# Kernel tuning notes

Measured on AMD Instinct MI355X. Metric: run time of the kernel, lower is better.

Reference implementation:

```python
import jax, jax.numpy as jnp
import numpy as np

GRID = 32            # grid_size -> num_locs = 1024
H, W = 8, 32         # ray panorama height/width
N_ANGLES = 360       # binned_rays: one bin per rounded degree


def _circ_conv(x, w, b, pad):
    # Conv2d with padding_mode='circular' (NCHW, OIHW)
    if pad > 0:
        x = jnp.pad(x, ((0, 0), (0, 0), (pad, pad), (pad, pad)), mode='wrap')
    y = jax.lax.conv_general_dilated(x, w, (1, 1), 'VALID',
                                     dimension_numbers=('NCHW', 'OIHW', 'NCHW'))
    return y + b[None, :, None, None]


def setup_inputs() -> dict:
    key = jax.random.key(0)
    ks = jax.random.split(key, 8)
    B, N, F, Co = 2, 20, 128, 64
    bbox = jax.random.uniform(ks[0], (B, 4), dtype=jnp.float32)
    near_locs = jax.random.uniform(ks[1], (B, N, 2), dtype=jnp.float32)
    near_feats = jax.random.normal(ks[2], (B, N, F, H, W), dtype=jnp.float32)
    overhead_feat = jax.random.normal(ks[3], (B, Co, GRID, GRID), dtype=jnp.float32)
    rays = jax.random.normal(ks[4], (N_ANGLES, 3, H, W), dtype=jnp.float32)
    cin = 8  # 1 dist + 3 orient + 2 pano stats + 2 overhead stats
    W1 = jax.random.normal(ks[5], (1, cin, 3, 3), dtype=jnp.float32) * 0.1
    b1 = jnp.zeros((1,), jnp.float32)
    W2 = jax.random.normal(ks[6], (1, cin, 5, 5), dtype=jnp.float32) * 0.1
    b2 = jnp.zeros((1,), jnp.float32)
    Wf = jax.random.normal(ks[7], (1, 2, 1, 1), dtype=jnp.float32) * 0.1
    bf = jnp.zeros((1,), jnp.float32)
    return dict(bbox=bbox, near_locs=near_locs, near_feats=near_feats,
                overhead_feat=overhead_feat, rays=rays,
                W1=W1, b1=b1, W2=W2, b2=b2, Wf=Wf, bf=bf)


def _grid_helper(bbox, near_locs):
    # grid-cell centers from bbox; D = euclidean dist, theta = bearing in [0, 2pi)
    ys = jnp.linspace(bbox[0], bbox[2], GRID)
    xs = jnp.linspace(bbox[1], bbox[3], GRID)
    gy, gx = jnp.meshgrid(ys, xs, indexing='ij')
    centers = jnp.stack([gy.ravel(), gx.ravel()], -1)              # [L,2]
    diff = near_locs[None, :, :] - centers[:, None, :]             # [L,N,2]
    D = jnp.sqrt(jnp.sum(diff * diff, -1))                         # [L,N]
    theta = jnp.mod(jnp.arctan2(diff[..., 1], diff[..., 0]), 2.0 * jnp.pi)
    return D, theta


def _one(bbox, near_locs, near_feats, overhead_feat, rays, W1, b1, W2, b2, Wf, bf):
    N, F = near_feats.shape[:2]
    L = GRID * GRID
    D, theta = _grid_helper(bbox, near_locs)
    theta_inds = jnp.mod(jnp.round(jnp.rad2deg(theta)).astype(jnp.int32), N_ANGLES)
    orientation = rays[theta_inds.reshape(-1)].reshape(L, N, 3, H, W)  # irregular gather
    distance = jnp.broadcast_to(D[:, :, None, None, None], (L, N, 1, H, W))
    # panorama stats: max/mean over channel dim of pano features
    pano_stats = jnp.stack([near_feats.max(1), near_feats.mean(1)], 1)  # [N,2,H,W]
    x_pano = jnp.broadcast_to(pano_stats[None], (L, N, 2, H, W))
    # overhead stats: flatten spatial -> (L, Co), max/mean over channels
    ov = overhead_feat.reshape(overhead_feat.shape[0], -1).T            # [L, Co]
    ov_stats = jnp.stack([ov.max(1), ov.mean(1)], 1)                    # [L,2]
    x_ov = jnp.broadcast_to(ov_stats[:, None, :, None, None], (L, N, 2, H, W))
    inp = jnp.concatenate([distance, orientation, x_pano, x_ov], 2)     # [L,N,8,H,W]
    x = inp.reshape(L * N, 8, H, W)
    c1 = _circ_conv(x, W1, b1, 1)
    c2 = _circ_conv(x, W2, b2, 2)
    fused = jnp.concatenate([c1, c2], 1)                                # [L*N,2,H,W]
    logits = _circ_conv(fused, Wf, bf, 0).reshape(L, N, H, W)
    weight = jax.nn.softmax(logits.reshape(L, -1), axis=1).reshape(L, N, H, W)
    tmp_feats = jnp.transpose(near_feats, (0, 2, 3, 1))                 # [N,H,W,F]
    grid_feats = jnp.einsum('pxyf,spxy->sf', tmp_feats, weight)         # [L,F]
    return (grid_feats.reshape(GRID, GRID, F),
            weight.reshape(GRID, GRID, N, H, W))


def reference(bbox, near_locs, near_feats, overhead_feat, rays, W1, b1, W2, b2, Wf, bf):
    fn = jax.vmap(_one, in_axes=(0, 0, 0, 0, None, None, None, None, None, None, None))
    return fn(bbox, near_locs, near_feats, overhead_feat, rays, W1, b1, W2, b2, Wf, bf)
```

## Files before the change

kernel.cpp:

```cpp
#include <hip/hip_runtime.h>
#include <hip/hip_fp16.h>
#include <math.h>

#define HH 8
#define WW 32
#define HW 256
#define NN 20
#define FF 128
#define LL 1024
#define AA 360
#define CO 64
#define KK 5120
#define KS 8
#define KC 640
#define BM 32
#define BK 64

#define OFF_LPANO      (AA*HW)
#define OFF_OV(B)      (OFF_LPANO + (B)*NN*HW)
#define OFF_SCAL(B)    (OFF_OV(B) + (B)*LL*2)
#define OFF_D(B)       (OFF_SCAL(B) + 8)
#define OFF_IDX(B)     (OFF_D(B) + (B)*LL*NN)
#define OFF_BASE2(B)   (OFF_IDX(B) + (B)*LL*NN)
#define OFF_MX(B)      (OFF_BASE2(B) + (B)*LL*NN)
#define OFF_INV(B)     (OFF_MX(B) + (B)*LL)
#define OFF_BT(B)      (((OFF_INV(B) + (B)*LL + 7)/8)*8)
#define OFF_CP(B)      (OFF_BT(B) + (B)*FF*KK/2)

typedef __attribute__((ext_vector_type(8))) _Float16 f16x8;
typedef __attribute__((ext_vector_type(4))) _Float16 f16x4;
typedef __attribute__((ext_vector_type(4))) float f32x4;

__global__ __launch_bounds__(256)
void kA_pre(const float* __restrict__ bbox, const float* __restrict__ locs,
            const float* __restrict__ rays, const float* __restrict__ feats,
            const float* __restrict__ overhead,
            const float* __restrict__ W1, const float* __restrict__ b1,
            const float* __restrict__ W2, const float* __restrict__ b2,
            const float* __restrict__ Wf, const float* __restrict__ bfp,
            float* __restrict__ ws, int B)
{
    const int bid = blockIdx.x, tid = threadIdx.x;
    const int g1 = AA + B*NN + B*4 + 1;
    const int gGeo = (B*LL*NN + 255)/256;

    if (bid < g1) {
        const float wf0 = Wf[0], wf1 = Wf[1];

        if (bid < AA) {
            __shared__ float s[3*HW];
            for (int c = 0; c < 3; ++c) s[c*HW + tid] = rays[(bid*3 + c)*HW + tid];
            __syncthreads();
            const int h = tid >> 5, w = tid & 31;
            float c1 = 0.f, c2 = 0.f;
            #pragma unroll
            for (int c = 0; c < 3; ++c) {
                #pragma unroll
                for (int ky = 0; ky < 3; ++ky)
                    #pragma unroll
                    for (int kx = 0; kx < 3; ++kx)
                        c1 += W1[(1+c)*9 + ky*3 + kx] *
                              s[c*HW + (((h+ky+7)&7)<<5) + ((w+kx+31)&31)];
                #pragma unroll
                for (int ky = 0; ky < 5; ++ky)
                    #pragma unroll
                    for (int kx = 0; kx < 5; ++kx)
                        c2 += W2[(1+c)*25 + ky*5 + kx] *
                              s[c*HW + (((h+ky+6)&7)<<5) + ((w+kx+30)&31)];
            }
            ws[bid*HW + tid] = wf0*c1 + wf1*c2;
            return;
        }

        const int pb = bid - AA;
        if (pb < B*NN) {
            __shared__ float p[2*HW];
            const float* fp = feats + (size_t)pb * FF * HW + tid;
            float mx = -INFINITY; double sm = 0.0;
            for (int f = 0; f < FF; ++f) {
                float v = fp[(size_t)f * HW];
                mx = fmaxf(mx, v); sm += (double)v;
            }
            p[tid]      = mx;
            p[HW + tid] = (float)(sm / 128.0);
            __syncthreads();
            const int h = tid >> 5, w = tid & 31;
            float c1 = 0.f, c2 = 0.f;
            #pragma unroll
            for (int c = 0; c < 2; ++c) {
                #pragma unroll
                for (int ky = 0; ky < 3; ++ky)
                    #pragma unroll
                    for (int kx = 0; kx < 3; ++kx)
                        c1 += W1[(4+c)*9 + ky*3 + kx] *
                              p[c*HW + (((h+ky+7)&7)<<5) + ((w+kx+31)&31)];
                #pragma unroll
                for (int ky = 0; ky < 5; ++ky)
                    #pragma unroll
                    for (int kx = 0; kx < 5; ++kx)
                        c2 += W2[(4+c)*25 + ky*5 + kx] *
                              p[c*HW + (((h+ky+6)&7)<<5) + ((w+kx+30)&31)];
            }
            ws[OFF_LPANO + pb*HW + tid] = wf0*c1 + wf1*c2;
            return;
        }

        const int ob = pb - B*NN;
        if (ob < B*4) {
            const int t = ob*256 + tid;
            const int b = t >> 10, l = t & 1023;
            const float* op = overhead + (size_t)b*CO*LL + l;
            float mx = -INFINITY; double sm = 0.0;
            for (int c = 0; c < CO; ++c) {
                float v = op[(size_t)c*LL];
                mx = fmaxf(mx, v); sm += (double)v;
            }
            ws[OFF_OV(B) + t*2]     = mx;
            ws[OFF_OV(B) + t*2 + 1] = (float)(sm / 64.0);
            return;
        }

        if (tid == 0) {
            double s10=0, s16=0, s17=0, s20=0, s26=0, s27=0;
            for (int i = 0; i < 9;  ++i) { s10 += W1[i]; s16 += W1[54+i];  s17 += W1[63+i]; }
            for (int i = 0; i < 25; ++i) { s20 += W2[i]; s26 += W2[150+i]; s27 += W2[175+i]; }
            ws[OFF_SCAL(B)+0] = (float)(wf0*s10 + wf1*s20);
            ws[OFF_SCAL(B)+1] = (float)(wf0*s16 + wf1*s26);
            ws[OFF_SCAL(B)+2] = (float)(wf0*s17 + wf1*s27);
            ws[OFF_SCAL(B)+3] = wf0*b1[0] + wf1*b2[0] + bfp[0];
        }
        return;
    }

    if (bid < g1 + gGeo) {
        const int t = (bid - g1)*256 + tid;
        if (t >= B*LL*NN) return;
        const int b = t / (LL*NN), r = t % (LL*NN), l = r / NN, n = r % NN;
        const int iy = l >> 5, ix = l & 31;
        const double y0 = (double)bbox[b*4+0], x0 = (double)bbox[b*4+1];
        const double y1 = (double)bbox[b*4+2], x1 = (double)bbox[b*4+3];
        const double cy = y0 + (double)iy * (y1 - y0) / 31.0;
        const double cx = x0 + (double)ix * (x1 - x0) / 31.0;
        const double d0 = (double)locs[(b*NN+n)*2+0] - cy;
        const double d1 = (double)locs[(b*NN+n)*2+1] - cx;
        const double D  = sqrt(d0*d0 + d1*d1);
        double th = atan2(d1, d0);
        const double TWO_PI = 6.283185307179586476925286766559;
        th -= TWO_PI * floor(th / TWO_PI);
        const double deg = th * 57.295779513082320876798154814105;
        int k = (int)llrint(deg);
        int idx = k % 360; if (idx < 0) idx += 360;
        ws[OFF_D(B) + t] = (float)D;
        ((int*)(ws + OFF_IDX(B)))[t] = idx;
        return;
    }

    {
        const int NG_PER_B = NN*FF*64;
        const int g = (bid - g1 - gGeo)*256 + tid;
        if (g >= B*NG_PER_B) return;
        const int b = g / NG_PER_B;
        const int r = g - b*NG_PER_B;
        const int n = r / (FF*64);
        const int r2 = r % (FF*64);
        const int f = r2 >> 6;
        const int hw0 = (r2 & 63) << 2;
        const float4 v = *(const float4*)(feats + ((size_t)((b*NN + n)*FF + f))*HW + hw0);
        f16x4 h;
        h[0] = (_Float16)v.x; h[1] = (_Float16)v.y;
        h[2] = (_Float16)v.z; h[3] = (_Float16)v.w;
        _Float16* bt = (_Float16*)(ws + OFF_BT(B));
        *(f16x4*)(bt + ((size_t)(b*FF + f))*KK + n*HW + hw0) = h;
    }
}

__global__ __launch_bounds__(256)
void kB_stats(float* __restrict__ ws, int B)
{
    const int bid = blockIdx.x, tid = threadIdx.x;
    const int b = bid / LL;
    const float* Lray  = ws;
    const float* Lpano = ws + OFF_LPANO;

    __shared__ float sb[NN];
    __shared__ int   si[NN];
    __shared__ float sred[8];
    if (tid < NN) {
        const float Dv = ws[OFF_D(B) + (size_t)bid*NN + tid];
        const int   ix = ((const int*)(ws + OFF_IDX(B)))[(size_t)bid*NN + tid];
        const float Cd  = ws[OFF_SCAL(B)+0], Com = ws[OFF_SCAL(B)+1];
        const float Cov = ws[OFF_SCAL(B)+2], Cb  = ws[OFF_SCAL(B)+3];
        const float bv = Cd*Dv + Com*ws[OFF_OV(B)+bid*2]
                       + Cov*ws[OFF_OV(B)+bid*2+1] + Cb;
        sb[tid] = bv; si[tid] = ix;
        ws[OFF_BASE2(B) + (size_t)bid*NN + tid] = bv;
    }
    __syncthreads();

    float lg[NN];
    float mx = -INFINITY;
    #pragma unroll
    for (int n = 0; n < NN; ++n) {
        lg[n] = sb[n] + Lray[si[n]*HW + tid] + Lpano[(b*NN+n)*HW + tid];
        mx = fmaxf(mx, lg[n]);
    }
    #pragma unroll
    for (int o = 32; o > 0; o >>= 1) mx = fmaxf(mx, __shfl_xor(mx, o, 64));
    if ((tid & 63) == 0) sred[tid >> 6] = mx;
    __syncthreads();
    mx = fmaxf(fmaxf(sred[0], sred[1]), fmaxf(sred[2], sred[3]));

    float sm = 0.f;
    #pragma unroll
    for (int n = 0; n < NN; ++n) sm += expf(lg[n] - mx);
    #pragma unroll
    for (int o = 32; o > 0; o >>= 1) sm += __shfl_xor(sm, o, 64);
    if ((tid & 63) == 0) sred[4 + (tid >> 6)] = sm;
    __syncthreads();
    if (tid == 0) {
        ws[OFF_MX(B)  + bid] = mx;
        ws[OFF_INV(B) + bid] = 1.0f / (sred[4] + sred[5] + sred[6] + sred[7]);
    }
}

__global__ __launch_bounds__(256)
void kC_gemm(const float* __restrict__ ws, float* __restrict__ wout,
             float* __restrict__ cp, int B)
{
    __shared__ __align__(16) _Float16 As[BM*BK];
    __shared__ __align__(16) _Float16 Bs[FF*BK];
    __shared__ float smx[BM], sinv[BM], sbase[BM*3];
    __shared__ int   sidx2[BM*3];

    const int x = blockIdx.x;
    const int ks = x & 7, mb = (x >> 3) & 31, b = x >> 8;
    const int l0 = mb * BM;
    const int kc0 = ks * KC;
    const int n0 = kc0 >> 8;
    const int bl0 = b*LL + l0;
    const int tid = threadIdx.x;
    const int wid = tid >> 6, lane = tid & 63, lr = lane & 15, lk = lane >> 4;

    if (tid < BM) {
        smx[tid]  = ws[OFF_MX(B)  + bl0 + tid];
        sinv[tid] = ws[OFF_INV(B) + bl0 + tid];
    } else if (tid >= 64 && tid < 64 + BM*3) {
        const int t = tid - 64;
        const int row = t/3, jj = t - row*3, n = n0 + jj;
        float bv = 0.f; int ix = 0;
        if (n < NN) {
            bv = ws[OFF_BASE2(B) + (size_t)(bl0 + row)*NN + n];
            ix = ((const int*)(ws + OFF_IDX(B)))[(size_t)(bl0 + row)*NN + n];
        }
        sbase[t] = bv; sidx2[t] = ix;
    }

    const _Float16* Btb = (const _Float16*)(ws + OFF_BT(B)) + (size_t)b*FF*KK;

    f32x4 acc[2][2] = {};

    int aoff[2][2], boff[2][2];
    #pragma unroll
    for (int m = 0; m < 2; ++m)
        #pragma unroll
        for (int kk = 0; kk < 2; ++kk) {
            const int row = m*16 + lr;
            aoff[m][kk] = row*128 + ((kk*64 + lk*16) ^ ((row & 7) << 4));
        }
    #pragma unroll
    for (int n = 0; n < 2; ++n)
        #pragma unroll
        for (int kk = 0; kk < 2; ++kk) {
            const int row = wid*32 + n*16 + lr;
            boff[n][kk] = row*128 + ((kk*64 + lk*16) ^ ((row & 7) << 4));
        }

    const int arow = tid >> 3, ac8 = tid & 7;
    const int adst = arow*128 + ((ac8*16) ^ ((arow & 7) << 4));

    char* AsB = (char*)As;
    char* BsB = (char*)Bs;

    __syncthreads();

    for (int s = 0; s < KC/BK; ++s) {
        const int kc = kc0 + s*BK;
        const int n = kc >> 8, jj = n - n0;
        {
            const int hwt = (kc & 255) + ac8*8;
            const float* lrp = ws + (size_t)sidx2[arow*3 + jj]*HW + hwt;
            const float* lpp = ws + OFF_LPANO + (size_t)(b*NN + n)*HW + hwt;
            const float bb = sbase[arow*3 + jj];
            const float m  = smx[arow];
            const float iv = sinv[arow];
            const float4 r0 = *(const float4*)lrp;
            const float4 r1 = *(const float4*)(lrp + 4);
            const float4 p0 = *(const float4*)lpp;
            const float4 p1 = *(const float4*)(lpp + 4);
            float w0 = expf(((bb + r0.x) + p0.x) - m) * iv;
            float w1 = expf(((bb + r0.y) + p0.y) - m) * iv;
            float w2 = expf(((bb + r0.z) + p0.z) - m) * iv;
            float w3 = expf(((bb + r0.w) + p0.w) - m) * iv;
            float w4 = expf(((bb + r1.x) + p1.x) - m) * iv;
            float w5 = expf(((bb + r1.y) + p1.y) - m) * iv;
            float w6 = expf(((bb + r1.z) + p1.z) - m) * iv;
            float w7 = expf(((bb + r1.w) + p1.w) - m) * iv;
            float* wp = wout + (size_t)(bl0 + arow)*KK + kc + ac8*8;
            const float4 o0 = {w0, w1, w2, w3};
            const float4 o1 = {w4, w5, w6, w7};
            *(float4*)wp = o0;
            *(float4*)(wp + 4) = o1;
            f16x8 h;
            h[0] = (_Float16)w0; h[1] = (_Float16)w1;
            h[2] = (_Float16)w2; h[3] = (_Float16)w3;
            h[4] = (_Float16)w4; h[5] = (_Float16)w5;
            h[6] = (_Float16)w6; h[7] = (_Float16)w7;
            *(f16x8*)(AsB + adst) = h;
        }
        #pragma unroll
        for (int c = 0; c < 4; ++c) {
            const int e = c*256 + tid;
            const int row = e >> 3, c8 = e & 7;
            const f16x8 h = *(const f16x8*)(Btb + (size_t)row*KK + kc + c8*8);
            const int dst = row*128 + ((c8*16) ^ ((row & 7) << 4));
            *(f16x8*)(BsB + dst) = h;
        }
        __syncthreads();
        #pragma unroll
        for (int kk = 0; kk < 2; ++kk) {
            const f16x8 a0 = *(const f16x8*)(AsB + aoff[0][kk]);
            const f16x8 a1 = *(const f16x8*)(AsB + aoff[1][kk]);
            const f16x8 b0 = *(const f16x8*)(BsB + boff[0][kk]);
            const f16x8 b1 = *(const f16x8*)(BsB + boff[1][kk]);
            acc[0][0] = __builtin_amdgcn_mfma_f32_16x16x32_f16(a0, b0, acc[0][0], 0, 0, 0);
            acc[0][1] = __builtin_amdgcn_mfma_f32_16x16x32_f16(a0, b1, acc[0][1], 0, 0, 0);
            acc[1][0] = __builtin_amdgcn_mfma_f32_16x16x32_f16(a1, b0, acc[1][0], 0, 0, 0);
            acc[1][1] = __builtin_amdgcn_mfma_f32_16x16x32_f16(a1, b1, acc[1][1], 0, 0, 0);
        }
        __syncthreads();
    }

    float* cpb = cp + ((size_t)ks*B*LL + (size_t)bl0)*FF;
    #pragma unroll
    for (int m = 0; m < 2; ++m)
        #pragma unroll
        for (int n = 0; n < 2; ++n) {
            const int col = wid*32 + n*16 + lr;
            #pragma unroll
            for (int r = 0; r < 4; ++r) {
                const int row = m*16 + lk*4 + r;
                cpb[(size_t)row*FF + col] = acc[m][n][r];
            }
        }
}

__global__ __launch_bounds__(256)
void kD_reduce(const float* __restrict__ cp, float* __restrict__ gout, int B)
{
    const size_t total = (size_t)B*LL*FF;
    const size_t i = ((size_t)blockIdx.x*256 + threadIdx.x)*4;
    if (i >= total) return;
    float4 s = {0.f, 0.f, 0.f, 0.f};
    #pragma unroll
    for (int ks = 0; ks < KS; ++ks) {
        const float4 v = *(const float4*)(cp + ks*total + i);
        s.x += v.x; s.y += v.y; s.z += v.z; s.w += v.w;
    }
    *(float4*)(gout + i) = s;
}

extern "C" void kernel_launch(void* const* d_in, const int* in_sizes, int n_in,
                              void* d_out, int out_size, void* d_ws, size_t ws_size,
                              hipStream_t stream)
{
    const float* bbox  = (const float*)d_in[0];
    const float* locs  = (const float*)d_in[1];
    const float* feats = (const float*)d_in[2];
    const float* over  = (const float*)d_in[3];
    const float* rays  = (const float*)d_in[4];
    const float* W1    = (const float*)d_in[5];
    const float* b1    = (const float*)d_in[6];
    const float* W2    = (const float*)d_in[7];
    const float* b2    = (const float*)d_in[8];
    const float* Wf    = (const float*)d_in[9];
    const float* bfp   = (const float*)d_in[10];
    const int B = in_sizes[0] / 4;
    float* ws  = (float*)d_ws;
    float* out = (float*)d_out;
    float* wout = out + (size_t)B*LL*FF;
    float* cp   = ws + OFF_CP(B);

    const int g1   = AA + B*NN + B*4 + 1;
    const int gGeo = (B*LL*NN + 255)/256;
    const int gBt  = (B*NN*FF*64)/256;

    kA_pre<<<dim3(g1 + gGeo + gBt), dim3(256), 0, stream>>>(
        bbox, locs, rays, feats, over, W1, b1, W2, b2, Wf, bfp, ws, B);
    kB_stats<<<dim3(B*LL), dim3(256), 0, stream>>>(ws, B);
    kC_gemm<<<dim3(B*32*KS), dim3(256), 0, stream>>>(ws, wout, cp, B);
    kD_reduce<<<dim3((B*LL*FF/4 + 255)/256), dim3(256), 0, stream>>>(cp, out, B);
}
```

Before: 43.64 us.

## Pre-swizzle B operand into MFMA fragment order and load directly from global

```diff
diff --git a/kernel.cpp b/kernel.cpp
--- a/kernel.cpp
+++ b/kernel.cpp
@@ -156,21 +156,24 @@
     }
 
     {
-        const int NG_PER_B = NN*FF*64;
-        const int g = (bid - g1 - gGeo)*256 + tid;
-        if (g >= B*NG_PER_B) return;
-        const int b = g / NG_PER_B;
-        const int r = g - b*NG_PER_B;
-        const int n = r / (FF*64);
-        const int r2 = r % (FF*64);
-        const int f = r2 >> 6;
-        const int hw0 = (r2 & 63) << 2;
-        const float4 v = *(const float4*)(feats + ((size_t)((b*NN + n)*FF + f))*HW + hw0);
-        f16x4 h;
-        h[0] = (_Float16)v.x; h[1] = (_Float16)v.y;
-        h[2] = (_Float16)v.z; h[3] = (_Float16)v.w;
-        _Float16* bt = (_Float16*)(ws + OFF_BT(B));
-        *(f16x4*)(bt + ((size_t)(b*FF + f))*KK + n*HW + hw0) = h;
+        const int t = (bid - g1 - gGeo)*256 + tid;
+        if (t >= B*FF*KK/8) return;
+        const int r  = t & 3;
+        const int f  = (t >> 2) & 127;
+        const int q  = (t >> 9) % 160;
+        const int b  = (t >> 9) / 160;
+        const int K8 = q*4 + r;
+        const int n   = K8 >> 5;
+        const int hw8 = K8 & 31;
+        const float* src = feats + ((size_t)((b*NN + n)*FF + f))*HW + hw8*8;
+        const float4 v0 = *(const float4*)src;
+        const float4 v1 = *(const float4*)(src + 4);
+        f16x8 h;
+        h[0] = (_Float16)v0.x; h[1] = (_Float16)v0.y;
+        h[2] = (_Float16)v0.z; h[3] = (_Float16)v0.w;
+        h[4] = (_Float16)v1.x; h[5] = (_Float16)v1.y;
+        h[6] = (_Float16)v1.z; h[7] = (_Float16)v1.w;
+        ((f16x8*)(ws + OFF_BT(B)))[t] = h;
     }
 }
 
@@ -227,8 +230,7 @@
 void kC_gemm(const float* __restrict__ ws, float* __restrict__ wout,
              float* __restrict__ cp, int B)
 {
-    __shared__ __align__(16) _Float16 As[BM*BK];
-    __shared__ __align__(16) _Float16 Bs[FF*BK];
+    __shared__ __align__(16) _Float16 As[BM*KC];
     __shared__ float smx[BM], sinv[BM], sbase[BM*3];
     __shared__ int   sidx2[BM*3];
 
@@ -254,90 +256,74 @@
         }
         sbase[t] = bv; sidx2[t] = ix;
     }
-
-    const _Float16* Btb = (const _Float16*)(ws + OFF_BT(B)) + (size_t)b*FF*KK;
-
-    f32x4 acc[2][2] = {};
-
-    int aoff[2][2], boff[2][2];
-    #pragma unroll
-    for (int m = 0; m < 2; ++m)
-        #pragma unroll
-        for (int kk = 0; kk < 2; ++kk) {
-            const int row = m*16 + lr;
-            aoff[m][kk] = row*128 + ((kk*64 + lk*16) ^ ((row & 7) << 4));
-        }
-    #pragma unroll
-    for (int n = 0; n < 2; ++n)
-        #pragma unroll
-        for (int kk = 0; kk < 2; ++kk) {
-            const int row = wid*32 + n*16 + lr;
-            boff[n][kk] = row*128 + ((kk*64 + lk*16) ^ ((row & 7) << 4));
-        }
-
+    __syncthreads();
+
+    char* AsB = (char*)As;
     const int arow = tid >> 3, ac8 = tid & 7;
-    const int adst = arow*128 + ((ac8*16) ^ ((arow & 7) << 4));
-
-    char* AsB = (char*)As;
-    char* BsB = (char*)Bs;
-
-    __syncthreads();
+    const float m_  = smx[arow];
+    const float iv_ = sinv[arow];
 
     for (int s = 0; s < KC/BK; ++s) {
         const int kc = kc0 + s*BK;
         const int n = kc >> 8, jj = n - n0;
-        {
-            const int hwt = (kc & 255) + ac8*8;
-            const float* lrp = ws + (size_t)sidx2[arow*3 + jj]*HW + hwt;
-            const float* lpp = ws + OFF_LPANO + (size_t)(b*NN + n)*HW + hwt;
-            const float bb = sbase[arow*3 + jj];
-            const float m  = smx[arow];
-            const float iv = sinv[arow];
-            const float4 r0 = *(const float4*)lrp;
-            const float4 r1 = *(const float4*)(lrp + 4);
-            const float4 p0 = *(const float4*)lpp;
-            const float4 p1 = *(const float4*)(lpp + 4);
-            float w0 = expf(((bb + r0.x) + p0.x) - m) * iv;
-            float w1 = expf(((bb + r0.y) + p0.y) - m) * iv;
-            float w2 = expf(((bb + r0.z) + p0.z) - m) * iv;
-            float w3 = expf(((bb + r0.w) + p0.w) - m) * iv;
-            float w4 = expf(((bb + r1.x) + p1.x) - m) * iv;
-            float w5 = expf(((bb + r1.y) + p1.y) - m) * iv;
-            float w6 = expf(((bb + r1.z) + p1.z) - m) * iv;
-            float w7 = expf(((bb + r1.w) + p1.w) - m) * iv;
-            float* wp = wout + (size_t)(bl0 + arow)*KK + kc + ac8*8;
-            const float4 o0 = {w0, w1, w2, w3};
-            const float4 o1 = {w4, w5, w6, w7};
-            *(float4*)wp = o0;
-            *(float4*)(wp + 4) = o1;
-            f16x8 h;
-            h[0] = (_Float16)w0; h[1] = (_Float16)w1;
-            h[2] = (_Float16)w2; h[3] = (_Float16)w3;
-            h[4] = (_Float16)w4; h[5] = (_Float16)w5;
-            h[6] = (_Float16)w6; h[7] = (_Float16)w7;
-            *(f16x8*)(AsB + adst) = h;
-        }
-        #pragma unroll
-        for (int c = 0; c < 4; ++c) {
-            const int e = c*256 + tid;
-            const int row = e >> 3, c8 = e & 7;
-            const f16x8 h = *(const f16x8*)(Btb + (size_t)row*KK + kc + c8*8);
-            const int dst = row*128 + ((c8*16) ^ ((row & 7) << 4));
-            *(f16x8*)(BsB + dst) = h;
-        }
-        __syncthreads();
+        const int hwt = (kc & 255) + ac8*8;
+        const float* lrp = ws + (size_t)sidx2[arow*3 + jj]*HW + hwt;
+        const float* lpp = ws + OFF_LPANO + (size_t)(b*NN + n)*HW + hwt;
+        const float bb = sbase[arow*3 + jj];
+        const float4 r0 = *(const float4*)lrp;
+        const float4 r1 = *(const float4*)(lrp + 4);
+        const float4 p0 = *(const float4*)lpp;
+        const float4 p1 = *(const float4*)(lpp + 4);
+        float w0 = expf(((bb + r0.x) + p0.x) - m_) * iv_;
+        float w1 = expf(((bb + r0.y) + p0.y) - m_) * iv_;
+        float w2 = expf(((bb + r0.z) + p0.z) - m_) * iv_;
+        float w3 = expf(((bb + r0.w) + p0.w) - m_) * iv_;
+        float w4 = expf(((bb + r1.x) + p1.x) - m_) * iv_;
+        float w5 = expf(((bb + r1.y) + p1.y) - m_) * iv_;
+        float w6 = expf(((bb + r1.z) + p1.z) - m_) * iv_;
+        float w7 = expf(((bb + r1.w) + p1.w) - m_) * iv_;
+        float* wp = wout + (size_t)(bl0 + arow)*KK + kc + ac8*8;
+        const float4 o0 = {w0, w1, w2, w3};
+        const float4 o1 = {w4, w5, w6, w7};
+        *(float4*)wp = o0;
+        *(float4*)(wp + 4) = o1;
+        f16x8 h;
+        h[0] = (_Float16)w0; h[1] = (_Float16)w1;
+        h[2] = (_Float16)w2; h[3] = (_Float16)w3;
+        h[4] = (_Float16)w4; h[5] = (_Float16)w5;
+        h[6] = (_Float16)w6; h[7] = (_Float16)w7;
+        const int dst = arow*1280 + ((s*128 + ac8*16) ^ ((arow & 7) << 4));
+        *(f16x8*)(AsB + dst) = h;
+    }
+    __syncthreads();
+
+    const f16x8* Bt2 = (const f16x8*)(ws + OFF_BT(B)) + (size_t)b*FF*KK/8;
+
+    f32x4 acc[2][2] = {};
+    for (int s = 0; s < KC/BK; ++s) {
+        f16x8 bf[2][2], af[2][2];
         #pragma unroll
         for (int kk = 0; kk < 2; ++kk) {
-            const f16x8 a0 = *(const f16x8*)(AsB + aoff[0][kk]);
-            const f16x8 a1 = *(const f16x8*)(AsB + aoff[1][kk]);
-            const f16x8 b0 = *(const f16x8*)(BsB + boff[0][kk]);
-            const f16x8 b1 = *(const f16x8*)(BsB + boff[1][kk]);
-            acc[0][0] = __builtin_amdgcn_mfma_f32_16x16x32_f16(a0, b0, acc[0][0], 0, 0, 0);
-            acc[0][1] = __builtin_amdgcn_mfma_f32_16x16x32_f16(a0, b1, acc[0][1], 0, 0, 0);
-            acc[1][0] = __builtin_amdgcn_mfma_f32_16x16x32_f16(a1, b0, acc[1][0], 0, 0, 0);
-            acc[1][1] = __builtin_amdgcn_mfma_f32_16x16x32_f16(a1, b1, acc[1][1], 0, 0, 0);
-        }
-        __syncthreads();
+            const int g = ks*20 + s*2 + kk;
+            #pragma unroll
+            for (int n = 0; n < 2; ++n)
+                bf[n][kk] = Bt2[(size_t)((g*128 + wid*32 + n*16 + lr) << 2) + lk];
+        }
+        #pragma unroll
+        for (int m = 0; m < 2; ++m)
+            #pragma unroll
+            for (int kk = 0; kk < 2; ++kk) {
+                const int row = m*16 + lr;
+                const int off = row*1280 + ((s*128 + kk*64 + lk*16) ^ ((lr & 7) << 4));
+                af[m][kk] = *(const f16x8*)(AsB + off);
+            }
+        #pragma unroll
+        for (int kk = 0; kk < 2; ++kk) {
+            acc[0][0] = __builtin_amdgcn_mfma_f32_16x16x32_f16(af[0][kk], bf[0][kk], acc[0][0], 0, 0, 0);
+            acc[0][1] = __builtin_amdgcn_mfma_f32_16x16x32_f16(af[0][kk], bf[1][kk], acc[0][1], 0, 0, 0);
+            acc[1][0] = __builtin_amdgcn_mfma_f32_16x16x32_f16(af[1][kk], bf[0][kk], acc[1][0], 0, 0, 0);
+            acc[1][1] = __builtin_amdgcn_mfma_f32_16x16x32_f16(af[1][kk], bf[1][kk], acc[1][1], 0, 0, 0);
+        }
     }
 
     float* cpb = cp + ((size_t)ks*B*LL + (size_t)bl0)*FF;
@@ -392,7 +378,7 @@
 
     const int g1   = AA + B*NN + B*4 + 1;
     const int gGeo = (B*LL*NN + 255)/256;
-    const int gBt  = (B*NN*FF*64)/256;
+    const int gBt  = (B*FF*KK/8 + 255)/256;
 
     kA_pre<<<dim3(g1 + gGeo + gBt), dim3(256), 0, stream>>>(
         bbox, locs, rays, feats, over, W1, b1, W2, b2, Wf, bfp, ws, B);
```

Measured after the change: 42.25 us. 1.03x faster.
